# Kernel tuning notes

Hardware: AMD Instinct MI355X
Metric: run time of the kernel (lower is better)

## Reference

```python
import jax, jax.numpy as jnp
import numpy as np

N, LATENT, HIDDEN, OUT, B = 65536, 128, 512, 64, 1024
W_WIDTH = 4.0  # LSH bucket width params['w']


def setup_inputs() -> dict:
    key = jax.random.key(0)
    ks = jax.random.split(key, 6)
    return {
        "z": jax.random.normal(ks[0], (N, LATENT), jnp.float32),
        "W1": jax.random.normal(ks[1], (LATENT, HIDDEN), jnp.float32) / np.float32(np.sqrt(LATENT)),
        "b1": jnp.zeros((HIDDEN,), jnp.float32),
        "W2": jax.random.normal(ks[2], (HIDDEN, OUT), jnp.float32) / np.float32(np.sqrt(HIDDEN)),
        "b2": jnp.zeros((OUT,), jnp.float32),
        "a": jax.random.normal(ks[3], (OUT,), jnp.float32),
        "lsh_b": jax.random.uniform(ks[4], (1,), jnp.float32) * W_WIDTH,
    }


def reference(z, W1, b1, W2, b2, a, lsh_b):
    # decoder MLP: latent -> hidden (relu) -> output_dim
    h = jax.nn.relu(z @ W1 + b1)
    x = h @ W2 + b2                                     # [N, OUT]
    # LSH random-projection hash: floor((x.a + b)/w), bucketed mod B
    code = jnp.floor((x @ a + lsh_b[0]) / W_WIDTH)
    bucket = jnp.mod(code.astype(jnp.int32), B)         # [N] segment ids
    # dict-based cluster grouping -> segmented mean per hash bucket
    sums = jax.ops.segment_sum(x, bucket, num_segments=B)                # [B, OUT]
    counts = jax.ops.segment_sum(jnp.ones((x.shape[0],), x.dtype), bucket, num_segments=B)
    means = sums / jnp.maximum(counts, 1.0)[:, None]    # [B, OUT]
    # squared distances point -> every cluster mean (gram trick, no [N,B,OUT] tensor)
    d2 = jnp.maximum(
        jnp.sum(x * x, -1)[:, None] + jnp.sum(means * means, -1)[None, :]
        - 2.0 * (x @ means.T),
        0.0)                                            # [N, B]
    # DEC-style Student-t soft cluster assignment
    q = 1.0 / (1.0 + d2)
    q_s = q / jnp.sum(q, -1, keepdims=True)
    return (q_s, means)
```

## Files before the change

### kernel.cpp

```cpp
#include <hip/hip_runtime.h>
#include <hip/hip_bf16.h>

#define N_PTS   65536
#define LATENT  128
#define HIDDEN  512
#define OUT_D   64
#define NBUCKET 1024
#define ROWS_A  32

typedef __attribute__((ext_vector_type(8))) short frag_ab;
typedef __attribute__((ext_vector_type(4))) float f32x4;

__device__ __forceinline__ short bf16h(float f) {
    union { float f; unsigned u; } c; c.f = f;
    const unsigned r = (c.u + 0x7FFFu + ((c.u >> 16) & 1u)) >> 16;
    return (short)r;
}
__device__ __forceinline__ float bf16tof(short s) {
    union { unsigned u; float f; } c; c.u = ((unsigned)(unsigned short)s) << 16;
    return c.f;
}
__device__ __forceinline__ float fbits(unsigned u) {
    union { unsigned u; float f; } c; c.u = u; return c.f;
}

__global__ __launch_bounds__(256) void prep_weights(
    const float* __restrict__ W1, const float* __restrict__ W2,
    short* __restrict__ wfrag)
{
    const int tid = blockIdx.x * 256 + threadIdx.x;
    const int c = tid / 1536;
    const int u = tid % 1536;
    frag_ab hi, lo;
    if (u < 1024) {
        const int l = u >> 4, slot = u & 15;
        const int j = slot ^ (l & 7);
        const int ct = j >> 3, ks = (j >> 1) & 3, hl = j & 1;
        const int n = (c * 2 + ct) * 16 + (l & 15);
        const int k0 = ks * 32 + ((l >> 4) << 3);
#pragma unroll
        for (int e = 0; e < 8; ++e) {
            const float wv = W1[(size_t)(k0 + e) * HIDDEN + n];
            const short h = bf16h(wv);
            hi[e] = h;
            lo[e] = bf16h(wv - bf16tof(h));
        }
        ((frag_ab*)wfrag)[(size_t)c * 1536 + u] = hl ? lo : hi;
    } else {
        const int u2 = u - 1024;
        const int l = u2 >> 3, slot = u2 & 7;
        const int j = slot ^ (l & 7);
        const int ot = j >> 1, hl = j & 1;
        const int n = ot * 16 + (l & 15);
#pragma unroll
        for (int e = 0; e < 8; ++e) {
            const int k = c * 32 + ((e >> 2) << 4) + ((l >> 4) << 2) + (e & 3);
            const float wv = W2[(size_t)k * OUT_D + n];
            const short h = bf16h(wv);
            hi[e] = h;
            lo[e] = bf16h(wv - bf16tof(h));
        }
        ((frag_ab*)wfrag)[(size_t)c * 1536 + u] = hl ? lo : hi;
    }
}

#define XP_STRIDE 512
#define BAND_U   5e-4f

__global__ __launch_bounds__(256, 2) void mlp_mfma_kernel(
    const float* __restrict__ z, const short* __restrict__ wfrag,
    const float* __restrict__ b1, const float* __restrict__ b2,
    const float* __restrict__ a, const float* __restrict__ lsh_b,
    short* __restrict__ xhi, short* __restrict__ xlo,
    float* __restrict__ xnorm_out, int* __restrict__ bucket_out,
    int* __restrict__ wsflag)
{
    __shared__ frag_ab LD[3072];
    short* LDs = (short*)LD;
    const int t = threadIdx.x;
    const int l = t & 63, w = t >> 6;
    const int sw = l & 7;
    const int row0 = blockIdx.x * 128 + w * 32;
    const frag_ab* wg = (const frag_ab*)wfrag;

    frag_ab zh[2][4], zl[2][4];
#pragma unroll
    for (int rg = 0; rg < 2; ++rg)
#pragma unroll
        for (int ks = 0; ks < 4; ++ks) {
            const float* src = z + (size_t)(row0 + rg * 16 + (l & 15)) * LATENT
                             + ks * 32 + ((l >> 4) << 3);
            const float4 p0 = *(const float4*)src;
            const float4 p1 = *(const float4*)(src + 4);
            const float v[8] = {p0.x, p0.y, p0.z, p0.w, p1.x, p1.y, p1.z, p1.w};
#pragma unroll
            for (int e = 0; e < 8; ++e) {
                const short h = bf16h(v[e]);
                zh[rg][ks][e] = h;
                zl[rg][ks][e] = bf16h(v[e] - bf16tof(h));
            }
        }

    f32x4 acc2[2][4];
#pragma unroll
    for (int rg = 0; rg < 2; ++rg)
#pragma unroll
        for (int ot = 0; ot < 4; ++ot) acc2[rg][ot] = (f32x4){0.f, 0.f, 0.f, 0.f};

#pragma unroll
    for (int i = 0; i < 6; ++i)
        __builtin_amdgcn_global_load_lds(
            (const __attribute__((address_space(1))) void*)(wg + (w * 6 + i) * 64 + l),
            (__attribute__((address_space(3))) void*)(&LD[(w * 6 + i) * 64]),
            16, 0, 0);
    __syncthreads();

#pragma unroll 1
    for (int c = 0; c < 16; ++c) {
        const int pb = (c & 1) * 1536;
        const int sb = 1536 - pb;
        if (c < 15) {
#pragma unroll
            for (int i = 0; i < 6; ++i)
                __builtin_amdgcn_global_load_lds(
                    (const __attribute__((address_space(1))) void*)(wg + (size_t)(c + 1) * 1536 + (w * 6 + i) * 64 + l),
                    (__attribute__((address_space(3))) void*)(&LD[sb + (w * 6 + i) * 64]),
                    16, 0, 0);
        }

        f32x4 acc1[2][2];
#pragma unroll
        for (int ct_l = 0; ct_l < 2; ++ct_l) {
            frag_ab bh[4], bl[4];
#pragma unroll
            for (int ks = 0; ks < 4; ++ks) {
                bh[ks] = LD[pb + l * 16 + ct_l * 8 + ((ks * 2) ^ sw)];
                bl[ks] = LD[pb + l * 16 + ct_l * 8 + ((ks * 2 + 1) ^ sw)];
            }
#pragma unroll
            for (int rg = 0; rg < 2; ++rg) {
                f32x4 acc = (f32x4){0.f, 0.f, 0.f, 0.f};
#pragma unroll
                for (int ks = 0; ks < 4; ++ks) {
                    acc = __builtin_amdgcn_mfma_f32_16x16x32_bf16(bh[ks], zh[rg][ks], acc, 0, 0, 0);
                    acc = __builtin_amdgcn_mfma_f32_16x16x32_bf16(bl[ks], zh[rg][ks], acc, 0, 0, 0);
                    acc = __builtin_amdgcn_mfma_f32_16x16x32_bf16(bh[ks], zl[rg][ks], acc, 0, 0, 0);
                }
                acc1[ct_l][rg] = acc;
            }
        }

        float4 b1v[2];
#pragma unroll
        for (int ct_l = 0; ct_l < 2; ++ct_l)
            b1v[ct_l] = *(const float4*)&b1[(c * 2 + ct_l) * 16 + ((l >> 4) << 2)];
        frag_ab ah2[2], al2[2];
#pragma unroll
        for (int rg = 0; rg < 2; ++rg)
#pragma unroll
            for (int e = 0; e < 8; ++e) {
                const int tile = e >> 2, r = e & 3;
                const float bb = (r == 0) ? b1v[tile].x : (r == 1) ? b1v[tile].y
                               : (r == 2) ? b1v[tile].z : b1v[tile].w;
                const float hv = fmaxf(acc1[tile][rg][r] + bb, 0.f);
                const short hh = bf16h(hv);
                ah2[rg][e] = hh;
                al2[rg][e] = bf16h(hv - bf16tof(hh));
            }

#pragma unroll
        for (int ot = 0; ot < 4; ++ot) {
            const frag_ab b2h = LD[pb + 1024 + l * 8 + ((ot * 2) ^ sw)];
            const frag_ab b2l = LD[pb + 1024 + l * 8 + ((ot * 2 + 1) ^ sw)];
#pragma unroll
            for (int rg = 0; rg < 2; ++rg) {
                acc2[rg][ot] = __builtin_amdgcn_mfma_f32_16x16x32_bf16(ah2[rg], b2h, acc2[rg][ot], 0, 0, 0);
                acc2[rg][ot] = __builtin_amdgcn_mfma_f32_16x16x32_bf16(al2[rg], b2h, acc2[rg][ot], 0, 0, 0);
                acc2[rg][ot] = __builtin_amdgcn_mfma_f32_16x16x32_bf16(ah2[rg], b2l, acc2[rg][ot], 0, 0, 0);
            }
        }
        __syncthreads();
    }

    float b2v[4], av[4];
#pragma unroll
    for (int ot = 0; ot < 4; ++ot) {
        b2v[ot] = b2[ot * 16 + (l & 15)];
        av[ot]  = a[ot * 16 + (l & 15)];
    }
    const int pbase = w * XP_STRIDE;
    int flagged = 0;
    const float lb = lsh_b[0];
#pragma unroll
    for (int rg = 0; rg < 2; ++rg)
#pragma unroll
        for (int r = 0; r < 4; ++r) {
            float sp = 0.f, np = 0.f;
            const int row_l = rg * 16 + (l >> 4) * 4 + r;
#pragma unroll
            for (int ot = 0; ot < 4; ++ot) {
                const float xv = acc2[rg][ot][r] + b2v[ot];
                sp = fmaf(xv, av[ot], sp);
                np = fmaf(xv, xv, np);
                const int col = ot * 16 + (l & 15);
                const short xh = bf16h(xv);
                LDs[(pbase + row_l * 8 + (col >> 3)) * 8 + (col & 7)] = xh;
                LDs[(pbase + 256 + row_l * 8 + (col >> 3)) * 8 + (col & 7)] = bf16h(xv - bf16tof(xh));
            }
#pragma unroll
            for (int off = 8; off >= 1; off >>= 1) {
                sp += __shfl_xor(sp, off, 16);
                np += __shfl_xor(np, off, 16);
            }
            if ((l & 15) == 0) {
                const int row = row0 + row_l;
                const float v = sp + lb;
                const float u = v * 0.25f;
                const float fl = floorf(u);
                bucket_out[row] = ((int)fl) & (NBUCKET - 1);
                xnorm_out[row] = np;
                const float fr = u - fl;
                if (fr < BAND_U || fr > 1.f - BAND_U) flagged = 1;
            }
        }
    const unsigned long long fb = __ballot(flagged != 0);
    if (l == 0) wsflag[blockIdx.x * 4 + w] = (fb != 0ull) ? 1 : 0;

    frag_ab* xhi8 = (frag_ab*)xhi;
    frag_ab* xlo8 = (frag_ab*)xlo;
#pragma unroll
    for (int j = 0; j < 4; ++j) {
        const int u = l + 64 * j;
        const size_t gidx = (size_t)(row0 + (u >> 3)) * 8 + (u & 7);
        xhi8[gidx] = LD[pbase + u];
        xlo8[gidx] = LD[pbase + 256 + u];
    }
}

__global__ __launch_bounds__(256, 3) void mlp_fixup_kernel(
    const float* __restrict__ z, const float* __restrict__ W1,
    const float* __restrict__ b1, const float* __restrict__ W2,
    const float* __restrict__ b2, const float* __restrict__ a,
    const float* __restrict__ lsh_b, const int* __restrict__ wsflag,
    short* __restrict__ xhi, short* __restrict__ xlo,
    float* __restrict__ xnorm_out, int* __restrict__ bucket_out)
{
    if (wsflag[blockIdx.x] == 0) return;
    __shared__ float zt[ROWS_A][LATENT];
    __shared__ float ht[ROWS_A][256];
    const int t = threadIdx.x;
    const int row0 = blockIdx.x * ROWS_A;

    {
        const float4* z4 = reinterpret_cast<const float4*>(z + (size_t)row0 * LATENT);
        float4* zt4 = reinterpret_cast<float4*>(&zt[0][0]);
#pragma unroll
        for (int i = 0; i < 4; ++i) zt4[t + 256 * i] = z4[t + 256 * i];
    }
    __syncthreads();

    const int tx = t & 63, ty = t >> 6;
    const int txq = t & 31, tyq = t >> 5;

    float acc2[4][2];
#pragma unroll
    for (int i = 0; i < 4; ++i) { acc2[i][0] = 0.f; acc2[i][1] = 0.f; }

    for (int h = 0; h < 2; ++h) {
        float acc1[8][4];
#pragma unroll
        for (int i = 0; i < 8; ++i)
#pragma unroll
            for (int cc = 0; cc < 4; ++cc) acc1[i][cc] = 0.f;

        const int jbase = h * 256 + tx;
#pragma unroll 2
        for (int k = 0; k < LATENT; k += 4) {
            float wv[4][4];
#pragma unroll
            for (int kk = 0; kk < 4; ++kk)
#pragma unroll
                for (int cc = 0; cc < 4; ++cc)
                    wv[kk][cc] = W1[(size_t)(k + kk) * HIDDEN + jbase + 64 * cc];
            float4 zv[8];
#pragma unroll
            for (int i = 0; i < 8; ++i)
                zv[i] = *reinterpret_cast<const float4*>(&zt[ty * 8 + i][k]);
#pragma unroll
            for (int i = 0; i < 8; ++i)
#pragma unroll
                for (int cc = 0; cc < 4; ++cc) {
                    acc1[i][cc] = fmaf(zv[i].x, wv[0][cc], acc1[i][cc]);
                    acc1[i][cc] = fmaf(zv[i].y, wv[1][cc], acc1[i][cc]);
                    acc1[i][cc] = fmaf(zv[i].z, wv[2][cc], acc1[i][cc]);
                    acc1[i][cc] = fmaf(zv[i].w, wv[3][cc], acc1[i][cc]);
                }
        }
        float bb[4];
#pragma unroll
        for (int cc = 0; cc < 4; ++cc) bb[cc] = b1[jbase + 64 * cc];
#pragma unroll
        for (int i = 0; i < 8; ++i)
#pragma unroll
            for (int cc = 0; cc < 4; ++cc)
                ht[ty * 8 + i][tx + 64 * cc] = fmaxf(acc1[i][cc] + bb[cc], 0.f);
        __syncthreads();

#pragma unroll 2
        for (int k = 0; k < 256; k += 4) {
            float w2v[4][2];
#pragma unroll
            for (int kk = 0; kk < 4; ++kk) {
                w2v[kk][0] = W2[(size_t)(h * 256 + k + kk) * OUT_D + txq];
                w2v[kk][1] = W2[(size_t)(h * 256 + k + kk) * OUT_D + txq + 32];
            }
            float4 hv[4];
#pragma unroll
            for (int i = 0; i < 4; ++i)
                hv[i] = *reinterpret_cast<const float4*>(&ht[tyq * 4 + i][k]);
#pragma unroll
            for (int i = 0; i < 4; ++i)
#pragma unroll
                for (int cc = 0; cc < 2; ++cc) {
                    acc2[i][cc] = fmaf(hv[i].x, w2v[0][cc], acc2[i][cc]);
                    acc2[i][cc] = fmaf(hv[i].y, w2v[1][cc], acc2[i][cc]);
                    acc2[i][cc] = fmaf(hv[i].z, w2v[2][cc], acc2[i][cc]);
                    acc2[i][cc] = fmaf(hv[i].w, w2v[3][cc], acc2[i][cc]);
                }
        }
        __syncthreads();
    }

    const float bb0 = b2[txq], bb1 = b2[txq + 32];
    const float a0 = a[txq], a1 = a[txq + 32];
    const float lb = lsh_b[0];
#pragma unroll
    for (int i = 0; i < 4; ++i) {
        const int row = row0 + tyq * 4 + i;
        const float x0 = acc2[i][0] + bb0;
        const float x1 = acc2[i][1] + bb1;
        const short h0 = bf16h(x0), h1 = bf16h(x1);
        xhi[(size_t)row * OUT_D + txq]      = h0;
        xhi[(size_t)row * OUT_D + txq + 32] = h1;
        xlo[(size_t)row * OUT_D + txq]      = bf16h(x0 - bf16tof(h0));
        xlo[(size_t)row * OUT_D + txq + 32] = bf16h(x1 - bf16tof(h1));

        float sa = fmaf(x0, a0, x1 * a1);
        float sn = fmaf(x0, x0, x1 * x1);
#pragma unroll
        for (int off = 16; off >= 1; off >>= 1) {
            sa += __shfl_xor(sa, off, 32);
            sn += __shfl_xor(sn, off, 32);
        }
        if (txq == 0) {
            const float code = floorf((sa + lb) * 0.25f);
            bucket_out[row] = ((int)code) & (NBUCKET - 1);
            xnorm_out[row] = sn;
        }
    }
}

__global__ __launch_bounds__(256) void hist_kernel(
    const int* __restrict__ bucket, int* __restrict__ blockhist,
    float* __restrict__ sums)
{
    __shared__ int h[NBUCKET];
    const int t = threadIdx.x, blk = blockIdx.x;
    for (int i = t; i < NBUCKET; i += 256) h[i] = 0;
    for (int i = t; i < NBUCKET; i += 256) sums[blk * NBUCKET + i] = 0.f;
    __syncthreads();
    const int rbase = blk * 1024;
#pragma unroll
    for (int i = 0; i < 4; ++i)
        atomicAdd(&h[bucket[rbase + i * 256 + t]], 1);
    __syncthreads();
    for (int i = t; i < NBUCKET; i += 256)
        blockhist[blk * NBUCKET + i] = h[i];
}

__global__ __launch_bounds__(1024) void scan_kernel(
    const int* __restrict__ blockhist, int* __restrict__ base,
    int* __restrict__ blockbase)
{
    __shared__ int sc[NBUCKET];
    const int b = threadIdx.x;
    int c = 0;
#pragma unroll 8
    for (int blk = 0; blk < 64; ++blk) c += blockhist[blk * NBUCKET + b];
    sc[b] = c;
    __syncthreads();
    for (int off = 1; off < NBUCKET; off <<= 1) {
        const int add = (b >= off) ? sc[b - off] : 0;
        __syncthreads();
        sc[b] += add;
        __syncthreads();
    }
    const int offset = sc[b] - c;
    base[b] = offset;
    if (b == NBUCKET - 1) base[NBUCKET] = offset + c;
    int run = offset;
#pragma unroll 4
    for (int blk = 0; blk < 64; ++blk) {
        blockbase[blk * NBUCKET + b] = run;
        run += blockhist[blk * NBUCKET + b];
    }
}

__global__ __launch_bounds__(256) void scatter_kernel(
    const int* __restrict__ bucket, const int* __restrict__ blockbase,
    int* __restrict__ order)
{
    __shared__ int lcur[NBUCKET];
    const int t = threadIdx.x, blk = blockIdx.x;
    for (int i = t; i < NBUCKET; i += 256) lcur[i] = 0;
    __syncthreads();
    const int rbase = blk * 1024;
#pragma unroll
    for (int i = 0; i < 4; ++i) {
        const int row = rbase + i * 256 + t;
        const int bk = bucket[row];
        const int r = atomicAdd(&lcur[bk], 1);
        order[blockbase[blk * NBUCKET + bk] + r] = row;
    }
}

__global__ __launch_bounds__(256) void chunksum_kernel(
    const short* __restrict__ xhi, const short* __restrict__ xlo,
    const int* __restrict__ order, const int* __restrict__ bucket,
    float* __restrict__ sums)
{
    const int t = threadIdx.x, lane = t & 63, w = t >> 6;
    const int c = blockIdx.x * 4 + w;
    const int i0 = c * 64;
    const int ordv = order[i0 + lane];
    const int bktv = bucket[ordv];
    float acc = 0.f;
    int cur = __shfl(bktv, 0, 64);
#pragma unroll 8
    for (int j = 0; j < 64; ++j) {
        const int rb = __shfl(ordv, j, 64);
        const int bb = __shfl(bktv, j, 64);
        if (bb != cur) {
            atomicAdd(&sums[(size_t)cur * OUT_D + lane], acc);
            acc = 0.f; cur = bb;
        }
        acc += bf16tof(xhi[(size_t)rb * OUT_D + lane])
             + bf16tof(xlo[(size_t)rb * OUT_D + lane]);
    }
    atomicAdd(&sums[(size_t)cur * OUT_D + lane], acc);
}

__global__ __launch_bounds__(64) void means_kernel(
    const float* __restrict__ sums, const int* __restrict__ base,
    float* __restrict__ means_out, float* __restrict__ mnorm,
    short* __restrict__ bfrag)
{
    const int b = blockIdx.x;
    const int k = threadIdx.x;
    const int cnt = base[b + 1] - base[b];
    const float m = sums[b * OUT_D + k] / fmaxf((float)cnt, 1.0f);
    means_out[b * OUT_D + k] = m;

    const short mh = bf16h(m);
    const short ml = bf16h(m - bf16tof(mh));
    const int tile = b >> 4, col = b & 15;
    const int lane = ((k & 31) >> 3) * 16 + col;
    const int f = (k >> 5) * 2;
    const size_t idx = ((size_t)(tile * 64 + lane) * 4 + f) * 8 + (k & 7);
    bfrag[idx] = mh;
    bfrag[idx + 8] = ml;

    float s = m * m;
#pragma unroll
    for (int off = 32; off >= 1; off >>= 1) s += __shfl_xor(s, off, 64);
    if (k == 0) mnorm[b] = s;
}

__global__ __launch_bounds__(256, 2) void q_kernel(
    const short* __restrict__ xhi, const short* __restrict__ xlo,
    const float* __restrict__ xnorm, const short* __restrict__ bfrag,
    const float* __restrict__ mnorm, float* __restrict__ q_out)
{
    __shared__ float rs_lds[4][2][16];
    const int t = threadIdx.x;
    const int l = t & 63;
    const int w = t >> 6;
    const int row0 = blockIdx.x * 32;
    const int lrow = (l >> 4) * 4;
    const int lcol = l & 15;

    const frag_ab* xh8 = reinterpret_cast<const frag_ab*>(xhi);
    const frag_ab* xl8 = reinterpret_cast<const frag_ab*>(xlo);
    frag_ab ah[2][2], al[2][2];
#pragma unroll
    for (int s = 0; s < 2; ++s)
#pragma unroll
        for (int kh = 0; kh < 2; ++kh) {
            const size_t idx8 = (size_t)(row0 + s * 16 + lcol) * 8 + kh * 4 + (l >> 4);
            ah[s][kh] = xh8[idx8];
            al[s][kh] = xl8[idx8];
        }

    float xn[2][4];
#pragma unroll
    for (int s = 0; s < 2; ++s)
#pragma unroll
        for (int r = 0; r < 4; ++r) xn[s][r] = xnorm[row0 + s * 16 + lrow + r];

    const frag_ab* bf8 = reinterpret_cast<const frag_ab*>(bfrag);
    unsigned qp[2][16][2];
    float rsp[2][4] = {{0.f,0.f,0.f,0.f},{0.f,0.f,0.f,0.f}};

#pragma unroll
    for (int j = 0; j < 16; ++j) {
        const int bt = w + 4 * j;
        const size_t bb = (size_t)(bt * 64 + l) * 4;
        const frag_ab b0h = bf8[bb + 0];
        const frag_ab b0l = bf8[bb + 1];
        const frag_ab b1h = bf8[bb + 2];
        const frag_ab b1l = bf8[bb + 3];
        const float mn = mnorm[bt * 16 + lcol];

#pragma unroll
        for (int s = 0; s < 2; ++s) {
            f32x4 acc = {0.f, 0.f, 0.f, 0.f};
            acc = __builtin_amdgcn_mfma_f32_16x16x32_bf16(ah[s][0], b0h, acc, 0, 0, 0);
            acc = __builtin_amdgcn_mfma_f32_16x16x32_bf16(ah[s][1], b1h, acc, 0, 0, 0);
            acc = __builtin_amdgcn_mfma_f32_16x16x32_bf16(ah[s][0], b0l, acc, 0, 0, 0);
            acc = __builtin_amdgcn_mfma_f32_16x16x32_bf16(ah[s][1], b1l, acc, 0, 0, 0);
            acc = __builtin_amdgcn_mfma_f32_16x16x32_bf16(al[s][0], b0h, acc, 0, 0, 0);
            acc = __builtin_amdgcn_mfma_f32_16x16x32_bf16(al[s][1], b1h, acc, 0, 0, 0);

            float qq[4];
#pragma unroll
            for (int r = 0; r < 4; ++r) {
                const float d2 = fmaxf(fmaf(-2.f, acc[r], xn[s][r] + mn), 0.f);
                qq[r] = __builtin_amdgcn_rcpf(1.f + d2);
                rsp[s][r] += qq[r];
            }
            qp[s][j][0] = ((unsigned)(unsigned short)bf16h(qq[1]) << 16)
                        | (unsigned)(unsigned short)bf16h(qq[0]);
            qp[s][j][1] = ((unsigned)(unsigned short)bf16h(qq[3]) << 16)
                        | (unsigned)(unsigned short)bf16h(qq[2]);
        }
    }

#pragma unroll
    for (int off = 8; off >= 1; off >>= 1)
#pragma unroll
        for (int s = 0; s < 2; ++s)
#pragma unroll
            for (int r = 0; r < 4; ++r) rsp[s][r] += __shfl_xor(rsp[s][r], off, 16);
    if (lcol == 0) {
#pragma unroll
        for (int s = 0; s < 2; ++s)
#pragma unroll
            for (int r = 0; r < 4; ++r) rs_lds[w][s][lrow + r] = rsp[s][r];
    }
    __syncthreads();

    float inv[2][4];
#pragma unroll
    for (int s = 0; s < 2; ++s)
#pragma unroll
        for (int r = 0; r < 4; ++r) {
            const float tot = rs_lds[0][s][lrow + r] + rs_lds[1][s][lrow + r]
                            + rs_lds[2][s][lrow + r] + rs_lds[3][s][lrow + r];
            inv[s][r] = __builtin_amdgcn_rcpf(tot);
        }

#pragma unroll
    for (int j = 0; j < 16; ++j) {
        const int col = (w + 4 * j) * 16 + lcol;
#pragma unroll
        for (int s = 0; s < 2; ++s) {
            const unsigned u0 = qp[s][j][0], u1 = qp[s][j][1];
            const float q0 = fbits(u0 << 16);
            const float q1 = fbits(u0 & 0xFFFF0000u);
            const float q2 = fbits(u1 << 16);
            const float q3 = fbits(u1 & 0xFFFF0000u);
            const size_t rb = (size_t)(row0 + s * 16 + lrow) * NBUCKET + col;
            __builtin_nontemporal_store(q0 * inv[s][0], &q_out[rb]);
            __builtin_nontemporal_store(q1 * inv[s][1], &q_out[rb + NBUCKET]);
            __builtin_nontemporal_store(q2 * inv[s][2], &q_out[rb + 2 * NBUCKET]);
            __builtin_nontemporal_store(q3 * inv[s][3], &q_out[rb + 3 * NBUCKET]);
        }
    }
}

extern "C" void kernel_launch(void* const* d_in, const int* in_sizes, int n_in,
                              void* d_out, int out_size, void* d_ws, size_t ws_size,
                              hipStream_t stream) {
    const float* z    = (const float*)d_in[0];
    const float* W1   = (const float*)d_in[1];
    const float* b1   = (const float*)d_in[2];
    const float* W2   = (const float*)d_in[3];
    const float* b2   = (const float*)d_in[4];
    const float* a    = (const float*)d_in[5];
    const float* lshb = (const float*)d_in[6];

    float* q_out     = (float*)d_out;
    float* means_out = q_out + (size_t)N_PTS * NBUCKET;

    char* ws = (char*)d_ws;
    short* xhi    = (short*)ws;
    short* xlo    = xhi + (size_t)N_PTS * OUT_D;
    short* bfrag  = xlo + (size_t)N_PTS * OUT_D;
    short* wfrag  = bfrag + (size_t)64 * 64 * 4 * 8;
    float* xnorm  = (float*)(wfrag + (size_t)16 * 1536 * 8);
    float* mnorm  = xnorm + N_PTS;
    float* sums   = mnorm + NBUCKET;
    int*   bucket = (int*)(sums + (size_t)NBUCKET * OUT_D);
    int*   order  = bucket + N_PTS;
    int*   blockhist = order + N_PTS;
    int*   blockbase = blockhist + 64 * NBUCKET;
    int*   base      = blockbase + 64 * NBUCKET;
    int*   wsflag    = base + NBUCKET + 1;

    prep_weights<<<96, 256, 0, stream>>>(W1, W2, wfrag);
    mlp_mfma_kernel<<<N_PTS / 128, 256, 0, stream>>>(z, wfrag, b1, b2, a, lshb,
                                                     xhi, xlo, xnorm, bucket, wsflag);
    mlp_fixup_kernel<<<N_PTS / ROWS_A, 256, 0, stream>>>(z, W1, b1, W2, b2, a, lshb, wsflag,
                                                         xhi, xlo, xnorm, bucket);
    hist_kernel<<<64, 256, 0, stream>>>(bucket, blockhist, sums);
    scan_kernel<<<1, 1024, 0, stream>>>(blockhist, base, blockbase);
    scatter_kernel<<<64, 256, 0, stream>>>(bucket, blockbase, order);
    chunksum_kernel<<<256, 256, 0, stream>>>(xhi, xlo, order, bucket, sums);
    means_kernel<<<NBUCKET, 64, 0, stream>>>(sums, base, means_out, mnorm, bfrag);
    q_kernel<<<N_PTS / 32, 256, 0, stream>>>(xhi, xlo, xnorm, bfrag, mnorm, q_out);
}
```

Baseline: 231.5 us.

## Recompute q in second pass instead of caching packed bf16 values; raise occupancy

The q kernel no longer keeps the 64 packed bf16 q values per lane in registers between the row-sum pass and the store pass. The second pass reloads the B fragments and redoes the MFMAs and reciprocals, and the launch bound rises to 3 blocks per SM to use the freed registers. This trades twice the MFMA work and fragment loads for lower register pressure and more waves to hide the store-bound output write. It also removes the bf16 rounding of stored q, which improves accuracy. Separately, the scan kernel caches its 64 block-histogram values in registers so they are read from memory only once.

Measured after the change: 294.6 us (median of 2 runs). +27.3%, slower.

```diff
diff --git a/kernel.cpp b/kernel.cpp
--- a/kernel.cpp
+++ b/kernel.cpp
@@ -19,9 +19,6 @@
 __device__ __forceinline__ float bf16tof(short s) {
     union { unsigned u; float f; } c; c.u = ((unsigned)(unsigned short)s) << 16;
     return c.f;
-}
-__device__ __forceinline__ float fbits(unsigned u) {
-    union { unsigned u; float f; } c; c.u = u; return c.f;
 }
 
 __global__ __launch_bounds__(256) void prep_weights(
@@ -384,9 +381,12 @@
 {
     __shared__ int sc[NBUCKET];
     const int b = threadIdx.x;
+    int vals[64];
+#pragma unroll
+    for (int blk = 0; blk < 64; ++blk) vals[blk] = blockhist[blk * NBUCKET + b];
     int c = 0;
-#pragma unroll 8
-    for (int blk = 0; blk < 64; ++blk) c += blockhist[blk * NBUCKET + b];
+#pragma unroll
+    for (int blk = 0; blk < 64; ++blk) c += vals[blk];
     sc[b] = c;
     __syncthreads();
     for (int off = 1; off < NBUCKET; off <<= 1) {
@@ -399,10 +399,10 @@
     base[b] = offset;
     if (b == NBUCKET - 1) base[NBUCKET] = offset + c;
     int run = offset;
-#pragma unroll 4
+#pragma unroll
     for (int blk = 0; blk < 64; ++blk) {
         blockbase[blk * NBUCKET + b] = run;
-        run += blockhist[blk * NBUCKET + b];
+        run += vals[blk];
     }
 }
 
@@ -476,7 +476,7 @@
     if (k == 0) mnorm[b] = s;
 }
 
-__global__ __launch_bounds__(256, 2) void q_kernel(
+__global__ __launch_bounds__(256, 3) void q_kernel(
     const short* __restrict__ xhi, const short* __restrict__ xlo,
     const float* __restrict__ xnorm, const short* __restrict__ bfrag,
     const float* __restrict__ mnorm, float* __restrict__ q_out)
@@ -508,7 +508,6 @@
         for (int r = 0; r < 4; ++r) xn[s][r] = xnorm[row0 + s * 16 + lrow + r];
 
     const frag_ab* bf8 = reinterpret_cast<const frag_ab*>(bfrag);
-    unsigned qp[2][16][2];
     float rsp[2][4] = {{0.f,0.f,0.f,0.f},{0.f,0.f,0.f,0.f}};
 
 #pragma unroll
@@ -530,18 +529,11 @@
             acc = __builtin_amdgcn_mfma_f32_16x16x32_bf16(ah[s][1], b1l, acc, 0, 0, 0);
             acc = __builtin_amdgcn_mfma_f32_16x16x32_bf16(al[s][0], b0h, acc, 0, 0, 0);
             acc = __builtin_amdgcn_mfma_f32_16x16x32_bf16(al[s][1], b1h, acc, 0, 0, 0);
-
-            float qq[4];
 #pragma unroll
             for (int r = 0; r < 4; ++r) {
                 const float d2 = fmaxf(fmaf(-2.f, acc[r], xn[s][r] + mn), 0.f);
-                qq[r] = __builtin_amdgcn_rcpf(1.f + d2);
-                rsp[s][r] += qq[r];
-            }
-            qp[s][j][0] = ((unsigned)(unsigned short)bf16h(qq[1]) << 16)
-                        | (unsigned)(unsigned short)bf16h(qq[0]);
-            qp[s][j][1] = ((unsigned)(unsigned short)bf16h(qq[3]) << 16)
-                        | (unsigned)(unsigned short)bf16h(qq[2]);
+                rsp[s][r] += __builtin_amdgcn_rcpf(1.f + d2);
+            }
         }
     }
 
@@ -571,19 +563,32 @@
 
 #pragma unroll
     for (int j = 0; j < 16; ++j) {
-        const int col = (w + 4 * j) * 16 + lcol;
+        const int bt = w + 4 * j;
+        const size_t bb = (size_t)(bt * 64 + l) * 4;
+        const frag_ab b0h = bf8[bb + 0];
+        const frag_ab b0l = bf8[bb + 1];
+        const frag_ab b1h = bf8[bb + 2];
+        const frag_ab b1l = bf8[bb + 3];
+        const float mn = mnorm[bt * 16 + lcol];
+        const int col = bt * 16 + lcol;
+
 #pragma unroll
         for (int s = 0; s < 2; ++s) {
-            const unsigned u0 = qp[s][j][0], u1 = qp[s][j][1];
-            const float q0 = fbits(u0 << 16);
-            const float q1 = fbits(u0 & 0xFFFF0000u);
-            const float q2 = fbits(u1 << 16);
-            const float q3 = fbits(u1 & 0xFFFF0000u);
+            f32x4 acc = {0.f, 0.f, 0.f, 0.f};
+            acc = __builtin_amdgcn_mfma_f32_16x16x32_bf16(ah[s][0], b0h, acc, 0, 0, 0);
+            acc = __builtin_amdgcn_mfma_f32_16x16x32_bf16(ah[s][1], b1h, acc, 0, 0, 0);
+            acc = __builtin_amdgcn_mfma_f32_16x16x32_bf16(ah[s][0], b0l, acc, 0, 0, 0);
+            acc = __builtin_amdgcn_mfma_f32_16x16x32_bf16(ah[s][1], b1l, acc, 0, 0, 0);
+            acc = __builtin_amdgcn_mfma_f32_16x16x32_bf16(al[s][0], b0h, acc, 0, 0, 0);
+            acc = __builtin_amdgcn_mfma_f32_16x16x32_bf16(al[s][1], b1h, acc, 0, 0, 0);
+
             const size_t rb = (size_t)(row0 + s * 16 + lrow) * NBUCKET + col;
-            __builtin_nontemporal_store(q0 * inv[s][0], &q_out[rb]);
-            __builtin_nontemporal_store(q1 * inv[s][1], &q_out[rb + NBUCKET]);
-            __builtin_nontemporal_store(q2 * inv[s][2], &q_out[rb + 2 * NBUCKET]);
-            __builtin_nontemporal_store(q3 * inv[s][3], &q_out[rb + 3 * NBUCKET]);
+#pragma unroll
+            for (int r = 0; r < 4; ++r) {
+                const float d2 = fmaxf(fmaf(-2.f, acc[r], xn[s][r] + mn), 0.f);
+                const float qq = __builtin_amdgcn_rcpf(1.f + d2);
+                __builtin_nontemporal_store(qq * inv[s][r], &q_out[rb + (size_t)r * NBUCKET]);
+            }
         }
     }
 }
```
